# Performance work log

Measured on AMD Instinct MI355X. Metric: run time of the kernel, lower is better.

The kernel has to match this reference:

```python
import jax, jax.numpy as jnp
import numpy as np


def dct_mat(N):
    # Orthonormal DCT-II matrix D, so dct(x, norm='ortho') along an axis = D @ x.
    n = jnp.arange(N, dtype=jnp.float32)
    k = jnp.arange(N, dtype=jnp.float32)[:, None]
    M = jnp.cos(jnp.pi * (n + 0.5) * k / N)  # [N, N]
    s = jnp.full((N, 1), jnp.sqrt(2.0 / N), dtype=jnp.float32).at[0, 0].set(jnp.sqrt(1.0 / N))
    return M * s


SCALE = 2


def setup_inputs() -> dict:
    key = jax.random.key(0)
    k1, _ = jax.random.split(key)
    x_lowres = jax.random.normal(k1, (16, 256, 64, 64), dtype=jnp.float32)
    sparse_mask = jnp.ones((1, 256, 1, 1), dtype=jnp.float32)
    return {"x_lowres": x_lowres, "sparse_mask": sparse_mask}


def reference(x_lowres, sparse_mask):
    B, C, H, W = x_lowres.shape
    H2, W2 = H * SCALE, W * SCALE

    DH, DW = dct_mat(H), dct_mat(W)
    # 2D ortho DCT: transform along W, then along H
    c = jnp.einsum('bchw,lw->bchl', x_lowres, DW)
    c = jnp.einsum('kh,bchl->bckl', DH, c)

    # Zero-pad high frequencies (bottom/right) up to target size
    c_pad = jnp.pad(c, ((0, 0), (0, 0), (0, H2 - H), (0, W2 - W)))

    # F.interpolate of a [1,C,1,1] map to (H2,W2) with bilinear/align_corners=False
    # is spatially constant per channel -> plain broadcast multiply is exact.
    c_mod = c_pad * sparse_mask

    # 2D ortho IDCT (DCT-III) at upsampled size: x = D^T @ y @ D
    DH2, DW2 = dct_mat(H2), dct_mat(W2)
    r = jnp.einsum('kn,bckl->bcnl', DH2, c_mod)
    out = jnp.einsum('bcnl,lm->bcnm', r, DW2)
    return out
```

## Files before the change

### kernel.cpp

```cpp
#include <hip/hip_runtime.h>


typedef __attribute__((ext_vector_type(8))) _Float16 f16x8;
typedef __attribute__((ext_vector_type(4))) _Float16 f16x4;
typedef __attribute__((ext_vector_type(4))) float f32x4;

#define NSLICES 4096
#define MFMA16(A, B, C) __builtin_amdgcn_mfma_f32_16x16x32_f16((A), (B), (C), 0, 0, 0)

__global__ void build_ut(_Float16* __restrict__ uf) {
    const int idx = blockIdx.x * 256 + threadIdx.x;
    const int n = idx >> 6;
    const int h = idx & 63;
    const float s0 = 0.125f;
    const float sk = 0.17677669529663687f;
    const float t0 = 0.088388347648318447f;
    const float tk = 0.125f;
    float acc = s0 * t0;
    #pragma unroll 4
    for (int k = 1; k < 64; ++k) {
        float a = cospif((float)((2 * h + 1) * k) * (1.0f / 128.0f));
        float b = cospif((float)((2 * n + 1) * k) * (1.0f / 256.0f));
        acc = fmaf(sk * tk * a, b, acc);
    }
    _Float16 hi = (_Float16)acc;
    _Float16 lo = (_Float16)(acc - (float)hi);
    const int j = n >> 4;
    const int lane = (n & 15) + 16 * ((h >> 3) & 3);
    const int kk = h >> 5;
    const int t = h & 7;
    const int base = ((j * 2 + kk) * 2) * 512 + lane * 8 + t;
    uf[base] = hi;
    uf[base + 512] = lo;
}

__global__ __launch_bounds__(256, 4)
void dct_fsr(const float* __restrict__ x, const float* __restrict__ mask,
             const _Float16* __restrict__ uf, float* __restrict__ out) {
    __shared__ _Float16 sRh[128 * 72];
    __shared__ _Float16 sRl[128 * 72];

    const int tid = threadIdx.x;
    const int wid = tid >> 6;
    const int lane = tid & 63;
    const int l15 = lane & 15;
    const int lg = lane >> 4;
    const int slice = blockIdx.x;
    const float mval = mask[slice & 255];

    const f16x8* ufr = (const f16x8*)uf;

    const float* xp = x + (size_t)slice * 4096 + (16 * wid + l15) * 64 + 8 * lg;
    const float4 xa = *(const float4*)xp;
    const float4 xb = *(const float4*)(xp + 4);
    const float4 xc = *(const float4*)(xp + 32);
    const float4 xd = *(const float4*)(xp + 36);

    f16x8 ah0, al0, ah1, al1;
#define SPLIT(H, L, E, V)                      \
    {                                          \
        float y_ = (V) * mval;                 \
        _Float16 h_ = (_Float16)y_;            \
        H[E] = h_;                             \
        L[E] = (_Float16)(y_ - (float)h_);     \
    }
    SPLIT(ah0, al0, 0, xa.x) SPLIT(ah0, al0, 1, xa.y)
    SPLIT(ah0, al0, 2, xa.z) SPLIT(ah0, al0, 3, xa.w)
    SPLIT(ah0, al0, 4, xb.x) SPLIT(ah0, al0, 5, xb.y)
    SPLIT(ah0, al0, 6, xb.z) SPLIT(ah0, al0, 7, xb.w)
    SPLIT(ah1, al1, 0, xc.x) SPLIT(ah1, al1, 1, xc.y)
    SPLIT(ah1, al1, 2, xc.z) SPLIT(ah1, al1, 3, xc.w)
    SPLIT(ah1, al1, 4, xd.x) SPLIT(ah1, al1, 5, xd.y)
    SPLIT(ah1, al1, 6, xd.z) SPLIT(ah1, al1, 7, xd.w)
#undef SPLIT

    #pragma unroll
    for (int j = 0; j < 8; ++j) {
        const f16x8 bh0 = ufr[((j * 2 + 0) * 2 + 0) * 64 + lane];
        const f16x8 bl0 = ufr[((j * 2 + 0) * 2 + 1) * 64 + lane];
        const f16x8 bh1 = ufr[((j * 2 + 1) * 2 + 0) * 64 + lane];
        const f16x8 bl1 = ufr[((j * 2 + 1) * 2 + 1) * 64 + lane];
        f32x4 acc = {0.f, 0.f, 0.f, 0.f};
        acc = MFMA16(ah0, bh0, acc);
        acc = MFMA16(ah1, bh1, acc);
        acc = MFMA16(ah0, bl0, acc);
        acc = MFMA16(ah1, bl1, acc);
        acc = MFMA16(al0, bh0, acc);
        acc = MFMA16(al1, bh1, acc);
        const int m = 16 * j + l15;
        const int h0 = 16 * wid + 4 * lg;
        f16x4 rh, rl;
        #pragma unroll
        for (int r = 0; r < 4; ++r) {
            const float vv = acc[r];
            const _Float16 hi = (_Float16)vv;
            rh[r] = hi;
            rl[r] = (_Float16)(vv - (float)hi);
        }
        *(f16x4*)&sRh[m * 72 + h0] = rh;
        *(f16x4*)&sRl[m * 72 + h0] = rl;
    }
    __syncthreads();

    float* og = out + (size_t)slice * 16384;
    #pragma unroll
    for (int i = 0; i < 2; ++i) {
        const int ig = 2 * wid + i;
        const f16x8 Ah0 = ufr[((ig * 2 + 0) * 2 + 0) * 64 + lane];
        const f16x8 Al0 = ufr[((ig * 2 + 0) * 2 + 1) * 64 + lane];
        const f16x8 Ah1 = ufr[((ig * 2 + 1) * 2 + 0) * 64 + lane];
        const f16x8 Al1 = ufr[((ig * 2 + 1) * 2 + 1) * 64 + lane];
        float* orow = og + (size_t)(16 * ig + 4 * lg) * 128 + l15;
        #pragma unroll
        for (int j = 0; j < 8; ++j) {
            const int m = 16 * j + l15;
            const f16x8 bh0 = *(const f16x8*)&sRh[m * 72 + 0 + 8 * lg];
            const f16x8 bh1 = *(const f16x8*)&sRh[m * 72 + 32 + 8 * lg];
            const f16x8 bl0 = *(const f16x8*)&sRl[m * 72 + 0 + 8 * lg];
            const f16x8 bl1 = *(const f16x8*)&sRl[m * 72 + 32 + 8 * lg];
            f32x4 a = {0.f, 0.f, 0.f, 0.f};
            a = MFMA16(Ah0, bh0, a);
            a = MFMA16(Ah1, bh1, a);
            a = MFMA16(Ah0, bl0, a);
            a = MFMA16(Ah1, bl1, a);
            a = MFMA16(Al0, bh0, a);
            a = MFMA16(Al1, bh1, a);
            #pragma unroll
            for (int r = 0; r < 4; ++r)
                orow[(size_t)r * 128 + 16 * j] = a[r];
        }
    }
}

extern "C" void kernel_launch(void* const* d_in, const int* in_sizes, int n_in,
                              void* d_out, int out_size, void* d_ws, size_t ws_size,
                              hipStream_t stream) {
    const float* x = (const float*)d_in[0];
    const float* mask = (const float*)d_in[1];
    float* out = (float*)d_out;
    _Float16* uf = (_Float16*)d_ws;

    build_ut<<<32, 256, 0, stream>>>(uf);
    dct_fsr<<<NSLICES, 256, 0, stream>>>(x, mask, uf, out);
}
```

Before: 335.8 us.

## Split each slice across two blocks by output column half

Each 64x64 slice is now handled by two blocks, one per 64-column half of the 128-wide output. Each block computes only its half of the intermediate, which halves shared memory and allows launch bounds of 8 blocks per CU. The stage-2 coefficient loads for the first row group are also hoisted above the barrier so they overlap it. The cost is that both blocks reload and split the same input slice, doubling input reads and stage-1 input conversion work.

```diff
diff --git a/kernel.cpp b/kernel.cpp
--- a/kernel.cpp
+++ b/kernel.cpp
@@ -5,7 +5,7 @@
 typedef __attribute__((ext_vector_type(4))) _Float16 f16x4;
 typedef __attribute__((ext_vector_type(4))) float f32x4;
 
-#define NSLICES 4096
+#define NBLOCKS 8192
 #define MFMA16(A, B, C) __builtin_amdgcn_mfma_f32_16x16x32_f16((A), (B), (C), 0, 0, 0)
 
 __global__ void build_ut(_Float16* __restrict__ uf) {
@@ -34,18 +34,20 @@
     uf[base + 512] = lo;
 }
 
-__global__ __launch_bounds__(256, 4)
+__global__ __launch_bounds__(256, 8)
 void dct_fsr(const float* __restrict__ x, const float* __restrict__ mask,
              const _Float16* __restrict__ uf, float* __restrict__ out) {
-    __shared__ _Float16 sRh[128 * 72];
-    __shared__ _Float16 sRl[128 * 72];
+    __shared__ _Float16 sRh[64 * 72];
+    __shared__ _Float16 sRl[64 * 72];
 
     const int tid = threadIdx.x;
     const int wid = tid >> 6;
     const int lane = tid & 63;
     const int l15 = lane & 15;
     const int lg = lane >> 4;
-    const int slice = blockIdx.x;
+    const int bid = blockIdx.x;
+    const int slice = bid >> 1;
+    const int mh = bid & 1;
     const float mval = mask[slice & 255];
 
     const f16x8* ufr = (const f16x8*)uf;
@@ -75,11 +77,12 @@
 #undef SPLIT
 
     #pragma unroll
-    for (int j = 0; j < 8; ++j) {
-        const f16x8 bh0 = ufr[((j * 2 + 0) * 2 + 0) * 64 + lane];
-        const f16x8 bl0 = ufr[((j * 2 + 0) * 2 + 1) * 64 + lane];
-        const f16x8 bh1 = ufr[((j * 2 + 1) * 2 + 0) * 64 + lane];
-        const f16x8 bl1 = ufr[((j * 2 + 1) * 2 + 1) * 64 + lane];
+    for (int j = 0; j < 4; ++j) {
+        const int jm = 4 * mh + j;
+        const f16x8 bh0 = ufr[((jm * 2 + 0) * 2 + 0) * 64 + lane];
+        const f16x8 bl0 = ufr[((jm * 2 + 0) * 2 + 1) * 64 + lane];
+        const f16x8 bh1 = ufr[((jm * 2 + 1) * 2 + 0) * 64 + lane];
+        const f16x8 bl1 = ufr[((jm * 2 + 1) * 2 + 1) * 64 + lane];
         f32x4 acc = {0.f, 0.f, 0.f, 0.f};
         acc = MFMA16(ah0, bh0, acc);
         acc = MFMA16(ah1, bh1, acc);
@@ -100,36 +103,50 @@
         *(f16x4*)&sRh[m * 72 + h0] = rh;
         *(f16x4*)&sRl[m * 72 + h0] = rl;
     }
+
+    const int ig0 = 2 * wid;
+    const f16x8 A0h0 = ufr[((ig0 * 2 + 0) * 2 + 0) * 64 + lane];
+    const f16x8 A0l0 = ufr[((ig0 * 2 + 0) * 2 + 1) * 64 + lane];
+    const f16x8 A0h1 = ufr[((ig0 * 2 + 1) * 2 + 0) * 64 + lane];
+    const f16x8 A0l1 = ufr[((ig0 * 2 + 1) * 2 + 1) * 64 + lane];
+
     __syncthreads();
 
-    float* og = out + (size_t)slice * 16384;
-    #pragma unroll
-    for (int i = 0; i < 2; ++i) {
-        const int ig = 2 * wid + i;
-        const f16x8 Ah0 = ufr[((ig * 2 + 0) * 2 + 0) * 64 + lane];
-        const f16x8 Al0 = ufr[((ig * 2 + 0) * 2 + 1) * 64 + lane];
-        const f16x8 Ah1 = ufr[((ig * 2 + 1) * 2 + 0) * 64 + lane];
-        const f16x8 Al1 = ufr[((ig * 2 + 1) * 2 + 1) * 64 + lane];
-        float* orow = og + (size_t)(16 * ig + 4 * lg) * 128 + l15;
-        #pragma unroll
-        for (int j = 0; j < 8; ++j) {
-            const int m = 16 * j + l15;
-            const f16x8 bh0 = *(const f16x8*)&sRh[m * 72 + 0 + 8 * lg];
-            const f16x8 bh1 = *(const f16x8*)&sRh[m * 72 + 32 + 8 * lg];
-            const f16x8 bl0 = *(const f16x8*)&sRl[m * 72 + 0 + 8 * lg];
-            const f16x8 bl1 = *(const f16x8*)&sRl[m * 72 + 32 + 8 * lg];
-            f32x4 a = {0.f, 0.f, 0.f, 0.f};
-            a = MFMA16(Ah0, bh0, a);
-            a = MFMA16(Ah1, bh1, a);
-            a = MFMA16(Ah0, bl0, a);
-            a = MFMA16(Ah1, bl1, a);
-            a = MFMA16(Al0, bh0, a);
-            a = MFMA16(Al1, bh1, a);
-            #pragma unroll
-            for (int r = 0; r < 4; ++r)
-                orow[(size_t)r * 128 + 16 * j] = a[r];
-        }
+    float* og = out + (size_t)slice * 16384 + 64 * mh;
+#define STAGE2(AH0, AL0, AH1, AL1, IG)                                   \
+    {                                                                    \
+        float* orow = og + (size_t)(16 * (IG) + 4 * lg) * 128 + l15;     \
+        _Pragma("unroll")                                                \
+        for (int j = 0; j < 4; ++j) {                                    \
+            const int m = 16 * j + l15;                                  \
+            const f16x8 bh0 = *(const f16x8*)&sRh[m * 72 + 0 + 8 * lg];  \
+            const f16x8 bh1 = *(const f16x8*)&sRh[m * 72 + 32 + 8 * lg]; \
+            const f16x8 bl0 = *(const f16x8*)&sRl[m * 72 + 0 + 8 * lg];  \
+            const f16x8 bl1 = *(const f16x8*)&sRl[m * 72 + 32 + 8 * lg]; \
+            f32x4 a = {0.f, 0.f, 0.f, 0.f};                              \
+            a = MFMA16(AH0, bh0, a);                                     \
+            a = MFMA16(AH1, bh1, a);                                     \
+            a = MFMA16(AH0, bl0, a);                                     \
+            a = MFMA16(AH1, bl1, a);                                     \
+            a = MFMA16(AL0, bh0, a);                                     \
+            a = MFMA16(AL1, bh1, a);                                     \
+            _Pragma("unroll")                                            \
+            for (int r = 0; r < 4; ++r)                                  \
+                orow[(size_t)r * 128 + 16 * j] = a[r];                   \
+        }                                                                \
     }
+
+    STAGE2(A0h0, A0l0, A0h1, A0l1, ig0)
+
+    {
+        const int ig1 = 2 * wid + 1;
+        const f16x8 A1h0 = ufr[((ig1 * 2 + 0) * 2 + 0) * 64 + lane];
+        const f16x8 A1l0 = ufr[((ig1 * 2 + 0) * 2 + 1) * 64 + lane];
+        const f16x8 A1h1 = ufr[((ig1 * 2 + 1) * 2 + 0) * 64 + lane];
+        const f16x8 A1l1 = ufr[((ig1 * 2 + 1) * 2 + 1) * 64 + lane];
+        STAGE2(A1h0, A1l0, A1h1, A1l1, ig1)
+    }
+#undef STAGE2
 }
 
 extern "C" void kernel_launch(void* const* d_in, const int* in_sizes, int n_in,
@@ -141,5 +158,5 @@
     _Float16* uf = (_Float16*)d_ws;
 
     build_ut<<<32, 256, 0, stream>>>(uf);
-    dct_fsr<<<NSLICES, 256, 0, stream>>>(x, mask, uf, out);
+    dct_fsr<<<NBLOCKS, 256, 0, stream>>>(x, mask, uf, out);
 }
```

New measurement: 347.2 us. 3.4% more time.

## Process four slices per block with prefetch, hoisted U loads, and vectorized stores

Applied to the files above, without the earlier changes.

Each block now handles four consecutive slices. The second-stage U fragments are loaded once into registers, and the next slice's input is prefetched while the current slice is computed. The second-stage MFMA operands are swapped so each lane writes a contiguous float4 of output instead of scattered scalar stores. A custom barrier that waits on LDS counters replaces __syncthreads, and a second barrier guards the shared buffers before reuse. The cost is more registers, two barriers per slice, and a grid four times smaller.

```diff
diff --git a/kernel.cpp b/kernel.cpp
--- a/kernel.cpp
+++ b/kernel.cpp
@@ -5,7 +5,8 @@
 typedef __attribute__((ext_vector_type(4))) _Float16 f16x4;
 typedef __attribute__((ext_vector_type(4))) float f32x4;
 
-#define NSLICES 4096
+#define SLICES_PER_BLOCK 4
+#define NBLOCKS (4096 / SLICES_PER_BLOCK)
 #define MFMA16(A, B, C) __builtin_amdgcn_mfma_f32_16x16x32_f16((A), (B), (C), 0, 0, 0)
 
 __global__ void build_ut(_Float16* __restrict__ uf) {
@@ -34,6 +35,13 @@
     uf[base + 512] = lo;
 }
 
+__device__ __forceinline__ void barrier_lgkm() {
+    __builtin_amdgcn_sched_barrier(0);
+    asm volatile("s_waitcnt lgkmcnt(0)" ::: "memory");
+    __builtin_amdgcn_s_barrier();
+    __builtin_amdgcn_sched_barrier(0);
+}
+
 __global__ __launch_bounds__(256, 4)
 void dct_fsr(const float* __restrict__ x, const float* __restrict__ mask,
              const _Float16* __restrict__ uf, float* __restrict__ out) {
@@ -45,18 +53,35 @@
     const int lane = tid & 63;
     const int l15 = lane & 15;
     const int lg = lane >> 4;
-    const int slice = blockIdx.x;
-    const float mval = mask[slice & 255];
+    const int slice0 = blockIdx.x * SLICES_PER_BLOCK;
 
     const f16x8* ufr = (const f16x8*)uf;
 
-    const float* xp = x + (size_t)slice * 4096 + (16 * wid + l15) * 64 + 8 * lg;
-    const float4 xa = *(const float4*)xp;
-    const float4 xb = *(const float4*)(xp + 4);
-    const float4 xc = *(const float4*)(xp + 32);
-    const float4 xd = *(const float4*)(xp + 36);
+    f16x8 Uh[2][2], Ul[2][2];
+    #pragma unroll
+    for (int i = 0; i < 2; ++i) {
+        const int ig = 2 * wid + i;
+        #pragma unroll
+        for (int kk = 0; kk < 2; ++kk) {
+            Uh[i][kk] = ufr[((ig * 2 + kk) * 2 + 0) * 64 + lane];
+            Ul[i][kk] = ufr[((ig * 2 + kk) * 2 + 1) * 64 + lane];
+        }
+    }
 
-    f16x8 ah0, al0, ah1, al1;
+    float4 xa, xb, xc, xd;
+    {
+        const float* xp = x + (size_t)slice0 * 4096 + (16 * wid + l15) * 64 + 8 * lg;
+        xa = *(const float4*)xp;
+        xb = *(const float4*)(xp + 4);
+        xc = *(const float4*)(xp + 32);
+        xd = *(const float4*)(xp + 36);
+    }
+
+    for (int s = 0; s < SLICES_PER_BLOCK; ++s) {
+        const int slice = slice0 + s;
+        const float mval = mask[slice & 255];
+
+        f16x8 ah0, al0, ah1, al1;
 #define SPLIT(H, L, E, V)                      \
     {                                          \
         float y_ = (V) * mval;                 \
@@ -64,71 +89,77 @@
         H[E] = h_;                             \
         L[E] = (_Float16)(y_ - (float)h_);     \
     }
-    SPLIT(ah0, al0, 0, xa.x) SPLIT(ah0, al0, 1, xa.y)
-    SPLIT(ah0, al0, 2, xa.z) SPLIT(ah0, al0, 3, xa.w)
-    SPLIT(ah0, al0, 4, xb.x) SPLIT(ah0, al0, 5, xb.y)
-    SPLIT(ah0, al0, 6, xb.z) SPLIT(ah0, al0, 7, xb.w)
-    SPLIT(ah1, al1, 0, xc.x) SPLIT(ah1, al1, 1, xc.y)
-    SPLIT(ah1, al1, 2, xc.z) SPLIT(ah1, al1, 3, xc.w)
-    SPLIT(ah1, al1, 4, xd.x) SPLIT(ah1, al1, 5, xd.y)
-    SPLIT(ah1, al1, 6, xd.z) SPLIT(ah1, al1, 7, xd.w)
+        SPLIT(ah0, al0, 0, xa.x) SPLIT(ah0, al0, 1, xa.y)
+        SPLIT(ah0, al0, 2, xa.z) SPLIT(ah0, al0, 3, xa.w)
+        SPLIT(ah0, al0, 4, xb.x) SPLIT(ah0, al0, 5, xb.y)
+        SPLIT(ah0, al0, 6, xb.z) SPLIT(ah0, al0, 7, xb.w)
+        SPLIT(ah1, al1, 0, xc.x) SPLIT(ah1, al1, 1, xc.y)
+        SPLIT(ah1, al1, 2, xc.z) SPLIT(ah1, al1, 3, xc.w)
+        SPLIT(ah1, al1, 4, xd.x) SPLIT(ah1, al1, 5, xd.y)
+        SPLIT(ah1, al1, 6, xd.z) SPLIT(ah1, al1, 7, xd.w)
 #undef SPLIT
 
-    #pragma unroll
-    for (int j = 0; j < 8; ++j) {
-        const f16x8 bh0 = ufr[((j * 2 + 0) * 2 + 0) * 64 + lane];
-        const f16x8 bl0 = ufr[((j * 2 + 0) * 2 + 1) * 64 + lane];
-        const f16x8 bh1 = ufr[((j * 2 + 1) * 2 + 0) * 64 + lane];
-        const f16x8 bl1 = ufr[((j * 2 + 1) * 2 + 1) * 64 + lane];
-        f32x4 acc = {0.f, 0.f, 0.f, 0.f};
-        acc = MFMA16(ah0, bh0, acc);
-        acc = MFMA16(ah1, bh1, acc);
-        acc = MFMA16(ah0, bl0, acc);
-        acc = MFMA16(ah1, bl1, acc);
-        acc = MFMA16(al0, bh0, acc);
-        acc = MFMA16(al1, bh1, acc);
-        const int m = 16 * j + l15;
-        const int h0 = 16 * wid + 4 * lg;
-        f16x4 rh, rl;
         #pragma unroll
-        for (int r = 0; r < 4; ++r) {
-            const float vv = acc[r];
-            const _Float16 hi = (_Float16)vv;
-            rh[r] = hi;
-            rl[r] = (_Float16)(vv - (float)hi);
+        for (int j = 0; j < 8; ++j) {
+            const f16x8 bh0 = ufr[((j * 2 + 0) * 2 + 0) * 64 + lane];
+            const f16x8 bl0 = ufr[((j * 2 + 0) * 2 + 1) * 64 + lane];
+            const f16x8 bh1 = ufr[((j * 2 + 1) * 2 + 0) * 64 + lane];
+            const f16x8 bl1 = ufr[((j * 2 + 1) * 2 + 1) * 64 + lane];
+            f32x4 acc = {0.f, 0.f, 0.f, 0.f};
+            acc = MFMA16(ah0, bh0, acc);
+            acc = MFMA16(ah1, bh1, acc);
+            acc = MFMA16(ah0, bl0, acc);
+            acc = MFMA16(ah1, bl1, acc);
+            acc = MFMA16(al0, bh0, acc);
+            acc = MFMA16(al1, bh1, acc);
+            const int m = 16 * j + l15;
+            const int h0 = 16 * wid + 4 * lg;
+            f16x4 rh, rl;
+            #pragma unroll
+            for (int r = 0; r < 4; ++r) {
+                const float vv = acc[r];
+                const _Float16 hi = (_Float16)vv;
+                rh[r] = hi;
+                rl[r] = (_Float16)(vv - (float)hi);
+            }
+            *(f16x4*)&sRh[m * 72 + h0] = rh;
+            *(f16x4*)&sRl[m * 72 + h0] = rl;
         }
-        *(f16x4*)&sRh[m * 72 + h0] = rh;
-        *(f16x4*)&sRl[m * 72 + h0] = rl;
-    }
-    __syncthreads();
 
-    float* og = out + (size_t)slice * 16384;
-    #pragma unroll
-    for (int i = 0; i < 2; ++i) {
-        const int ig = 2 * wid + i;
-        const f16x8 Ah0 = ufr[((ig * 2 + 0) * 2 + 0) * 64 + lane];
-        const f16x8 Al0 = ufr[((ig * 2 + 0) * 2 + 1) * 64 + lane];
-        const f16x8 Ah1 = ufr[((ig * 2 + 1) * 2 + 0) * 64 + lane];
-        const f16x8 Al1 = ufr[((ig * 2 + 1) * 2 + 1) * 64 + lane];
-        float* orow = og + (size_t)(16 * ig + 4 * lg) * 128 + l15;
+        if (s + 1 < SLICES_PER_BLOCK) {
+            const float* xp =
+                x + (size_t)(slice + 1) * 4096 + (16 * wid + l15) * 64 + 8 * lg;
+            xa = *(const float4*)xp;
+            xb = *(const float4*)(xp + 4);
+            xc = *(const float4*)(xp + 32);
+            xd = *(const float4*)(xp + 36);
+        }
+
+        barrier_lgkm();
+
+        float* og = out + (size_t)slice * 16384;
         #pragma unroll
         for (int j = 0; j < 8; ++j) {
             const int m = 16 * j + l15;
-            const f16x8 bh0 = *(const f16x8*)&sRh[m * 72 + 0 + 8 * lg];
-            const f16x8 bh1 = *(const f16x8*)&sRh[m * 72 + 32 + 8 * lg];
-            const f16x8 bl0 = *(const f16x8*)&sRl[m * 72 + 0 + 8 * lg];
-            const f16x8 bl1 = *(const f16x8*)&sRl[m * 72 + 32 + 8 * lg];
-            f32x4 a = {0.f, 0.f, 0.f, 0.f};
-            a = MFMA16(Ah0, bh0, a);
-            a = MFMA16(Ah1, bh1, a);
-            a = MFMA16(Ah0, bl0, a);
-            a = MFMA16(Ah1, bl1, a);
-            a = MFMA16(Al0, bh0, a);
-            a = MFMA16(Al1, bh1, a);
+            const f16x8 rh0 = *(const f16x8*)&sRh[m * 72 + 0 + 8 * lg];
+            const f16x8 rh1 = *(const f16x8*)&sRh[m * 72 + 32 + 8 * lg];
+            const f16x8 rl0 = *(const f16x8*)&sRl[m * 72 + 0 + 8 * lg];
+            const f16x8 rl1 = *(const f16x8*)&sRl[m * 72 + 32 + 8 * lg];
             #pragma unroll
-            for (int r = 0; r < 4; ++r)
-                orow[(size_t)r * 128 + 16 * j] = a[r];
+            for (int i = 0; i < 2; ++i) {
+                f32x4 a = {0.f, 0.f, 0.f, 0.f};
+                a = MFMA16(rh0, Uh[i][0], a);
+                a = MFMA16(rh1, Uh[i][1], a);
+                a = MFMA16(rh0, Ul[i][0], a);
+                a = MFMA16(rh1, Ul[i][1], a);
+                a = MFMA16(rl0, Uh[i][0], a);
+                a = MFMA16(rl1, Uh[i][1], a);
+                *(f32x4*)&og[(size_t)(16 * (2 * wid + i) + l15) * 128 + 16 * j +
+                             4 * lg] = a;
+            }
         }
+
+        barrier_lgkm();
     }
 }
 
@@ -141,5 +172,5 @@
     _Float16* uf = (_Float16*)d_ws;
 
     build_ut<<<32, 256, 0, stream>>>(uf);
-    dct_fsr<<<NSLICES, 256, 0, stream>>>(x, mask, uf, out);
+    dct_fsr<<<NBLOCKS, 256, 0, stream>>>(x, mask, uf, out);
 }
```

Result: slower. 473.3 us (+40.9%).
